# Kernel optimization log

Hardware: AMD Instinct MI355X
Metric: run time of the kernel (lower is better)

## Reference

```python
import jax, jax.numpy as jnp
import numpy as np
from jax.scipy.special import logsumexp

D_MODEL = 512
NHEAD = 8
BATCH = 2
SEQ = 1024


def _safe_log_relu(v):
    # log(max(v, 0)) with well-defined (zero) gradient where v <= 0
    pos = v > 0
    return jnp.where(pos, jnp.log(jnp.where(pos, v, 1.0)), -jnp.inf)


def _split_heads(t, h):
    b, l, hd = t.shape
    return t.reshape(b, l, h, hd // h).transpose(0, 2, 1, 3)  # (B,H,L,d)


def setup_inputs() -> dict:
    key = jax.random.key(0)
    ks = jax.random.split(key, 9)
    s = 1.0 / np.sqrt(D_MODEL)
    x = jax.random.normal(ks[0], (BATCH, SEQ, D_MODEL), jnp.float32)
    mk = lambda k: jax.random.normal(k, (D_MODEL, D_MODEL), jnp.float32) * s
    mb = lambda k: jax.random.normal(k, (D_MODEL,), jnp.float32) * 0.02
    return {
        "x": x,
        "W_Q": mk(ks[1]), "b_Q": mb(ks[2]),
        "W_K": mk(ks[3]), "b_K": mb(ks[4]),
        "W_V": mk(ks[5]), "b_V": mb(ks[6]),
        "W_O": mk(ks[7]), "b_O": mb(ks[8]),
    }


def reference(x, W_Q, b_Q, W_K, b_K, W_V, b_V, W_O, b_O):
    # self-attention: queries = keys = values = x
    Q = _split_heads(x @ W_Q.T + b_Q, NHEAD)  # (B,H,L,D)
    K = _split_heads(x @ W_K.T + b_K, NHEAD)  # (B,H,L,D)
    V = _split_heads(x @ W_V.T + b_V, NHEAD)  # (B,H,L,Dv)

    # normalizer: log sum_j sum_d exp(Q_id) * exp(K_jd)
    log_B = logsumexp(Q + logsumexp(K, axis=-2, keepdims=True), axis=-1)  # (B,H,L)

    log_V_plus = _safe_log_relu(V)[..., None, :]    # (B,H,L,1,Dv)
    log_V_minus = _safe_log_relu(-V)[..., None, :]  # (B,H,L,1,Dv)

    # reduce over key positions: (B,H,L,D,Dv) -> (B,H,D,Dv)
    lse_KV_plus = logsumexp(K[..., :, :, None] + log_V_plus, axis=-3)
    lse_KV_minus = logsumexp(K[..., :, :, None] + log_V_minus, axis=-3)

    # reduce over feature dim D: (B,H,L,D,Dv) -> (B,H,L,Dv)
    log_A_plus = logsumexp(Q[..., None] + lse_KV_plus[..., None, :, :], axis=-2)
    log_A_minus = logsumexp(Q[..., None] + lse_KV_minus[..., None, :, :], axis=-2)

    heads = jnp.exp(log_A_plus - log_B[..., None]) - jnp.exp(log_A_minus - log_B[..., None])

    b, h, l, dv = heads.shape
    joined = heads.transpose(0, 2, 1, 3).reshape(b, l, h * dv)
    return joined @ W_O.T + b_O
```

## Files before the change

### kernel.cpp

```cpp
#include <hip/hip_runtime.h>
#include <math.h>

#define DM   512
#define NH   8
#define HD   64
#define B_   2
#define L_   1024
#define M_   (B_ * L_)

typedef __attribute__((ext_vector_type(8))) short  bfrag;
typedef __attribute__((ext_vector_type(4))) float  fv4;
typedef __attribute__((ext_vector_type(4))) unsigned short usv4;
typedef __attribute__((ext_vector_type(8))) unsigned short usv8;

__device__ __forceinline__ unsigned short f32_bf16_rne(float f) {
    unsigned u = __float_as_uint(f);
    unsigned r = u + 0x7FFF + ((u >> 16) & 1);
    return (unsigned short)(r >> 16);
}
__device__ __forceinline__ float bf16_f32(unsigned short h) {
    return __uint_as_float(((unsigned)h) << 16);
}

__device__ __forceinline__ void cvt8(const float4 a, const float4 b,
                                     usv8* hi, usv8* lo) {
    float f[8] = {a.x, a.y, a.z, a.w, b.x, b.y, b.z, b.w};
#pragma unroll
    for (int k = 0; k < 8; ++k) {
        unsigned short h = f32_bf16_rne(f[k]);
        (*hi)[k] = h;
        (*lo)[k] = f32_bf16_rne(f[k] - bf16_f32(h));
    }
}

__device__ __forceinline__ void stage16(const unsigned short* g, unsigned short* l) {
    __builtin_amdgcn_global_load_lds(
        (const __attribute__((address_space(1))) void*)g,
        (__attribute__((address_space(3))) void*)l,
        16, 0, 0);
}

#define TM 64
#define TN 64
#define TK 32
#define LDA 32
#define NSTEP (DM / TK)

__global__ __launch_bounds__(256) void gemm_qkv_kernel(
    const float* __restrict__ x,
    const float* __restrict__ Wq, const float* __restrict__ Wk,
    const float* __restrict__ Wv,
    const float* __restrict__ bq, const float* __restrict__ bk,
    const float* __restrict__ bv,
    float* __restrict__ Qe, float* __restrict__ Ke, float* __restrict__ V,
    float* __restrict__ zred) {
    __shared__ __align__(16) unsigned short Ah[2][TM * LDA];
    __shared__ __align__(16) unsigned short Al[2][TM * LDA];
    __shared__ __align__(16) unsigned short Bh[2][TN * LDA];
    __shared__ __align__(16) unsigned short Bl[2][TN * LDA];

    const int z = blockIdx.z;
    const float* W    = (z == 0) ? Wq : (z == 1) ? Wk : Wv;
    const float* bias = (z == 0) ? bq : (z == 1) ? bk : bv;
    float* C          = (z == 0) ? Qe : (z == 1) ? Ke : V;
    const int m0 = blockIdx.y * TM, n0 = blockIdx.x * TN;
    const int do_exp = (z < 2);

    const int tid = threadIdx.x;
    if (blockIdx.x == 0 && blockIdx.y == 0 && z == 0) {
        float4 zv = {0.f, 0.f, 0.f, 0.f};
        *(float4*)(zred + (size_t)tid * 4) = zv;
    }

    const int wave = tid >> 6, lane = tid & 63;
    const int quad = lane >> 4, r16 = lane & 15;
    const int srow = lane >> 2;
    const int scol = (lane & 3) << 3;
    const size_t gaBase = (size_t)(m0 + wave * 16 + srow) * DM + scol;
    const size_t gbBase = (size_t)(n0 + wave * 16 + srow) * DM + scol;
    const int soff = (wave * 16 + srow) * LDA + scol;

    fv4 acc[4] = {};

    {
        float4 a0 = *(const float4*)(x + gaBase);
        float4 a1 = *(const float4*)(x + gaBase + 4);
        float4 b0 = *(const float4*)(W + gbBase);
        float4 b1 = *(const float4*)(W + gbBase + 4);
        usv8 h, l;
        cvt8(a0, a1, &h, &l);
        *(usv8*)(&Ah[0][soff]) = h; *(usv8*)(&Al[0][soff]) = l;
        cvt8(b0, b1, &h, &l);
        *(usv8*)(&Bh[0][soff]) = h; *(usv8*)(&Bl[0][soff]) = l;
    }
    __syncthreads();

    int cur = 0;
    for (int t = 0; t < NSTEP; ++t) {
        float4 na0, na1, nb0, nb1;
        if (t + 1 < NSTEP) {
            const size_t k = (size_t)(t + 1) * TK;
            na0 = *(const float4*)(x + gaBase + k);
            na1 = *(const float4*)(x + gaBase + k + 4);
            nb0 = *(const float4*)(W + gbBase + k);
            nb1 = *(const float4*)(W + gbBase + k + 4);
        }
        const int aoff = (wave * 16 + r16) * LDA + quad * 8;
        bfrag ah = *(const bfrag*)(&Ah[cur][aoff]);
        bfrag al = *(const bfrag*)(&Al[cur][aoff]);
        bfrag bh[4], bl[4];
#pragma unroll
        for (int j = 0; j < 4; ++j) {
            const int boff = (j * 16 + r16) * LDA + quad * 8;
            bh[j] = *(const bfrag*)(&Bh[cur][boff]);
            bl[j] = *(const bfrag*)(&Bl[cur][boff]);
        }
#pragma unroll
        for (int j = 0; j < 4; ++j) {
            acc[j] = __builtin_amdgcn_mfma_f32_16x16x32_bf16(ah, bh[j], acc[j], 0, 0, 0);
            acc[j] = __builtin_amdgcn_mfma_f32_16x16x32_bf16(ah, bl[j], acc[j], 0, 0, 0);
            acc[j] = __builtin_amdgcn_mfma_f32_16x16x32_bf16(al, bh[j], acc[j], 0, 0, 0);
        }
        if (t + 1 < NSTEP) {
            usv8 h, l;
            cvt8(na0, na1, &h, &l);
            *(usv8*)(&Ah[cur ^ 1][soff]) = h; *(usv8*)(&Al[cur ^ 1][soff]) = l;
            cvt8(nb0, nb1, &h, &l);
            *(usv8*)(&Bh[cur ^ 1][soff]) = h; *(usv8*)(&Bl[cur ^ 1][soff]) = l;
        }
        __syncthreads();
        cur ^= 1;
    }

#pragma unroll
    for (int j = 0; j < 4; ++j) {
        int n = n0 + j * 16 + r16;
        float bn = bias[n];
#pragma unroll
        for (int r = 0; r < 4; ++r) {
            int m = m0 + wave * 16 + quad * 4 + r;
            float v = acc[j][r] + bn;
            if (do_exp) v = __expf(v);
            C[(size_t)m * DM + n] = v;
        }
    }
}

__global__ __launch_bounds__(256) void gemm_out_kernel(
    const unsigned short* __restrict__ jh, const unsigned short* __restrict__ jl,
    const unsigned short* __restrict__ w2h, const unsigned short* __restrict__ w2l,
    const float* __restrict__ bo, float* __restrict__ C) {
    __shared__ __align__(16) unsigned short Ah[2][TM * LDA];
    __shared__ __align__(16) unsigned short Al[2][TM * LDA];
    __shared__ __align__(16) unsigned short Bh[2][TN * LDA];
    __shared__ __align__(16) unsigned short Bl[2][TN * LDA];

    const int bb = blockIdx.y >> 4;
    const unsigned short* Ahg = jh;
    const unsigned short* Alg = jl;
    const unsigned short* Bhg = w2h + (size_t)bb * 262144;
    const unsigned short* Blg = w2l + (size_t)bb * 262144;
    const int m0 = blockIdx.y * TM, n0 = blockIdx.x * TN;

    const int tid  = threadIdx.x;
    const int wave = tid >> 6, lane = tid & 63;
    const int quad = lane >> 4, r16 = lane & 15;
    const int srow = lane >> 2;
    const int scol = (lane & 3) << 3;
    const size_t gaBase = (size_t)(m0 + wave * 16 + srow) * DM + scol;
    const size_t gbBase = (size_t)(n0 + wave * 16 + srow) * DM + scol;
    const int ldst = wave * 512;

    fv4 acc[4] = {};

    stage16(Ahg + gaBase, &Ah[0][ldst]);
    stage16(Alg + gaBase, &Al[0][ldst]);
    stage16(Bhg + gbBase, &Bh[0][ldst]);
    stage16(Blg + gbBase, &Bl[0][ldst]);
    __syncthreads();

    int cur = 0;
    for (int t = 0; t < NSTEP; ++t) {
        if (t + 1 < NSTEP) {
            const size_t koff = (size_t)(t + 1) * TK;
            stage16(Ahg + gaBase + koff, &Ah[cur ^ 1][ldst]);
            stage16(Alg + gaBase + koff, &Al[cur ^ 1][ldst]);
            stage16(Bhg + gbBase + koff, &Bh[cur ^ 1][ldst]);
            stage16(Blg + gbBase + koff, &Bl[cur ^ 1][ldst]);
        }
        const int aoff = (wave * 16 + r16) * LDA + quad * 8;
        bfrag ah = *(const bfrag*)(&Ah[cur][aoff]);
        bfrag al = *(const bfrag*)(&Al[cur][aoff]);
        bfrag bh[4], bl[4];
#pragma unroll
        for (int j = 0; j < 4; ++j) {
            const int boff = (j * 16 + r16) * LDA + quad * 8;
            bh[j] = *(const bfrag*)(&Bh[cur][boff]);
            bl[j] = *(const bfrag*)(&Bl[cur][boff]);
        }
#pragma unroll
        for (int j = 0; j < 4; ++j) {
            acc[j] = __builtin_amdgcn_mfma_f32_16x16x32_bf16(ah, bh[j], acc[j], 0, 0, 0);
            acc[j] = __builtin_amdgcn_mfma_f32_16x16x32_bf16(ah, bl[j], acc[j], 0, 0, 0);
            acc[j] = __builtin_amdgcn_mfma_f32_16x16x32_bf16(al, bh[j], acc[j], 0, 0, 0);
        }
        __syncthreads();
        cur ^= 1;
    }

#pragma unroll
    for (int j = 0; j < 4; ++j) {
        int n = n0 + j * 16 + r16;
        float bn = bo[n];
#pragma unroll
        for (int r = 0; r < 4; ++r) {
            int m = m0 + wave * 16 + quad * 4 + r;
            C[(size_t)m * DM + n] = acc[j][r] + bn;
        }
    }
}

#define JT 64
__global__ __launch_bounds__(256) void kv_stats_kernel(
    const float* __restrict__ Kbuf, const float* __restrict__ Vbuf,
    float* __restrict__ Spart, float* __restrict__ zred) {
    const int split = blockIdx.x, bh = blockIdx.y;
    const int b = bh >> 3, h = bh & 7;
    const int j0 = split * JT;

    __shared__ __align__(16) float EK[JT][HD + 4];
    __shared__ __align__(16) float VS[JT][HD + 4];

    const int tid = threadIdx.x;
#pragma unroll
    for (int t = 0; t < 4; ++t) {
        int idx = tid + t * 256;
        int r = idx >> 4;
        int c = (idx & 15) << 2;
        size_t row = (size_t)(b * L_ + j0 + r) * DM + h * HD + c;
        *(float4*)&EK[r][c] = *(const float4*)(Kbuf + row);
        *(float4*)&VS[r][c] = *(const float4*)(Vbuf + row);
    }
    __syncthreads();

    const int tx = tid & 15, ty = tid >> 4;
    float acc[4][4] = {{0.f}};
#pragma unroll 8
    for (int jj = 0; jj < JT; ++jj) {
        float4 ek = *(const float4*)&EK[jj][ty * 4];
        float4 vs = *(const float4*)&VS[jj][tx * 4];
        float e[4] = {ek.x, ek.y, ek.z, ek.w};
        float v[4] = {vs.x, vs.y, vs.z, vs.w};
#pragma unroll
        for (int i = 0; i < 4; ++i)
#pragma unroll
            for (int j = 0; j < 4; ++j) acc[i][j] += e[i] * v[j];
    }

    float* sp = Spart + ((size_t)bh * 16 + split) * (HD * HD);
#pragma unroll
    for (int i = 0; i < 4; ++i) {
        float4 o; o.x = acc[i][0]; o.y = acc[i][1]; o.z = acc[i][2]; o.w = acc[i][3];
        *(float4*)(sp + (ty * 4 + i) * HD + tx * 4) = o;
    }
    if (tid < HD) {
        float z = 0.f;
#pragma unroll 8
        for (int jj = 0; jj < JT; ++jj) z += EK[jj][tid];
        atomicAdd(zred + (size_t)bh * HD + tid, z);
    }
}

__global__ __launch_bounds__(256) void mid_kernel(
    const float* __restrict__ Spart, const float* __restrict__ zred,
    const float* __restrict__ Qbuf, const float* __restrict__ Wo,
    unsigned short* __restrict__ w2h, unsigned short* __restrict__ w2l,
    unsigned short* __restrict__ jh, unsigned short* __restrict__ jl) {
    const int tid = threadIdx.x;
    const int bid = blockIdx.x;
    if (bid < 128) {
        __shared__ __align__(16) float Sl[HD][HD + 4];
        __shared__ __align__(16) float Wol[HD][HD + 4];
        const int b = bid >> 6, r = bid & 63;
        const int h = r >> 3, nq = r & 7;
        const int n0 = nq * 64, bh = b * NH + h;
        const float* sp = Spart + (size_t)bh * 16 * (HD * HD);
#pragma unroll
        for (int t4 = 0; t4 < 4; ++t4) {
            int idx4 = tid + t4 * 256;
            const float* p0 = sp + (size_t)idx4 * 4;
            float4 s = {0.f, 0.f, 0.f, 0.f};
#pragma unroll
            for (int p = 0; p < 16; ++p) {
                float4 v = *(const float4*)(p0 + (size_t)p * (HD * HD));
                s.x += v.x; s.y += v.y; s.z += v.z; s.w += v.w;
            }
            int d = idx4 >> 4, e4 = (idx4 & 15) << 2;
            *(float4*)&Sl[d][e4] = s;
            *(float4*)&Wol[d][e4] =
                *(const float4*)(Wo + (size_t)(n0 + d) * DM + h * HD + e4);
        }
        __syncthreads();
        const int nl = tid & 15;
        const int d0 = tid >> 4;
        float acc[4][4] = {};
#pragma unroll
        for (int e4 = 0; e4 < 16; ++e4) {
            float4 w[4], s[4];
#pragma unroll
            for (int j = 0; j < 4; ++j) w[j] = *(const float4*)&Wol[nl + j * 16][e4 * 4];
#pragma unroll
            for (int i = 0; i < 4; ++i) s[i] = *(const float4*)&Sl[d0 + i * 16][e4 * 4];
#pragma unroll
            for (int j = 0; j < 4; ++j)
#pragma unroll
                for (int i = 0; i < 4; ++i)
                    acc[j][i] += w[j].x * s[i].x + w[j].y * s[i].y
                               + w[j].z * s[i].z + w[j].w * s[i].w;
        }
#pragma unroll
        for (int j = 0; j < 4; ++j) {
            int n = n0 + nl + j * 16;
#pragma unroll
            for (int i = 0; i < 4; ++i) {
                int d = d0 + i * 16;
                size_t addr = ((size_t)(b * DM + n)) * DM + h * HD + d;
                float v = acc[j][i];
                unsigned short hh = f32_bf16_rne(v);
                w2h[addr] = hh;
                w2l[addr] = f32_bf16_rne(v - bf16_f32(hh));
            }
        }
    } else {
        const int bid2 = bid - 128;
        const int w = tid >> 6, lane = tid & 63;
        const int b = bid2 >> 5;
        const int row0 = bid2 * 32 + w * 8;
        const float4 z0 = *(const float4*)(zred + (size_t)b * DM + lane * 8);
        const float4 z1 = *(const float4*)(zred + (size_t)b * DM + lane * 8 + 4);
#pragma unroll
        for (int rr = 0; rr < 8; ++rr) {
            const size_t rowoff = (size_t)(row0 + rr) * DM + lane * 8;
            float4 q0 = *(const float4*)(Qbuf + rowoff);
            float4 q1 = *(const float4*)(Qbuf + rowoff + 4);
            float part = q0.x * z0.x + q0.y * z0.y + q0.z * z0.z + q0.w * z0.w
                       + q1.x * z1.x + q1.y * z1.y + q1.z * z1.z + q1.w * z1.w;
            part += __shfl_xor(part, 1, 64);
            part += __shfl_xor(part, 2, 64);
            part += __shfl_xor(part, 4, 64);
            float inv = 1.0f / part;
            float v[8] = {q0.x * inv, q0.y * inv, q0.z * inv, q0.w * inv,
                          q1.x * inv, q1.y * inv, q1.z * inv, q1.w * inv};
            usv8 hv, lv;
#pragma unroll
            for (int k = 0; k < 8; ++k) {
                unsigned short hh = f32_bf16_rne(v[k]);
                hv[k] = hh;
                lv[k] = f32_bf16_rne(v[k] - bf16_f32(hh));
            }
            *(usv8*)(jh + rowoff) = hv;
            *(usv8*)(jl + rowoff) = lv;
        }
    }
}

extern "C" void kernel_launch(void* const* d_in, const int* in_sizes, int n_in,
                              void* d_out, int out_size, void* d_ws, size_t ws_size,
                              hipStream_t stream) {
    const float* x  = (const float*)d_in[0];
    const float* Wq = (const float*)d_in[1];
    const float* bq = (const float*)d_in[2];
    const float* Wk = (const float*)d_in[3];
    const float* bk = (const float*)d_in[4];
    const float* Wv = (const float*)d_in[5];
    const float* bv = (const float*)d_in[6];
    const float* Wo = (const float*)d_in[7];
    const float* bo = (const float*)d_in[8];
    float* out = (float*)d_out;

    float* f = (float*)d_ws;
    const size_t NQ = (size_t)M_ * DM;
    float* Qe    = f;
    float* Ke    = f + NQ;
    float* V     = f + 2 * NQ;
    float* Spart = f + 3 * NQ;
    float* zred  = f + 4 * NQ;
    unsigned short* u = (unsigned short*)(f + 4 * NQ + 1024);
    unsigned short* jh  = u;
    unsigned short* jl  = jh + NQ;
    unsigned short* w2h = jl + NQ;
    unsigned short* w2l = w2h + 524288;

    dim3 gQKV(DM / TN, M_ / TM, 3);
    gemm_qkv_kernel<<<gQKV, 256, 0, stream>>>(x, Wq, Wk, Wv, bq, bk, bv,
                                              Qe, Ke, V, zred);

    kv_stats_kernel<<<dim3(16, 16), 256, 0, stream>>>(Ke, V, Spart, zred);

    mid_kernel<<<192, 256, 0, stream>>>(Spart, zred, Qe, Wo, w2h, w2l, jh, jl);

    dim3 gO(DM / TN, M_ / TM, 1);
    gemm_out_kernel<<<gO, 256, 0, stream>>>(jh, jl, w2h, w2l, bo, out);
}
```

Baseline: 131.3 us.

## Fuse K column-sum into QKV GEMM epilogue and regroup middle kernels

The K column sums (zred) are now accumulated in the QKV GEMM epilogue through shared-memory and global atomics, so the stats kernel no longer reduces them. That lets the Q normalization and bf16 split move into the same launch as the K^T V partial products (kv_scale_kernel), while the Wo fold becomes its own kernel. Zeroing zred moves to a hipMemsetAsync. The aim is to shorten the critical path by running the Q scaling alongside the KV stats, at the cost of extra atomics in the GEMM epilogue and one more launch (the memset).

```diff
diff --git a/kernel.cpp b/kernel.cpp
--- a/kernel.cpp
+++ b/kernel.cpp
@@ -58,6 +58,7 @@
     __shared__ __align__(16) unsigned short Al[2][TM * LDA];
     __shared__ __align__(16) unsigned short Bh[2][TN * LDA];
     __shared__ __align__(16) unsigned short Bl[2][TN * LDA];
+    __shared__ float zl[TN];
 
     const int z = blockIdx.z;
     const float* W    = (z == 0) ? Wq : (z == 1) ? Wk : Wv;
@@ -65,13 +66,9 @@
     float* C          = (z == 0) ? Qe : (z == 1) ? Ke : V;
     const int m0 = blockIdx.y * TM, n0 = blockIdx.x * TN;
     const int do_exp = (z < 2);
-
-    const int tid = threadIdx.x;
-    if (blockIdx.x == 0 && blockIdx.y == 0 && z == 0) {
-        float4 zv = {0.f, 0.f, 0.f, 0.f};
-        *(float4*)(zred + (size_t)tid * 4) = zv;
-    }
-
+    const int do_z   = (z == 1);
+
+    const int tid  = threadIdx.x;
     const int wave = tid >> 6, lane = tid & 63;
     const int quad = lane >> 4, r16 = lane & 15;
     const int srow = lane >> 2;
@@ -79,6 +76,8 @@
     const size_t gaBase = (size_t)(m0 + wave * 16 + srow) * DM + scol;
     const size_t gbBase = (size_t)(n0 + wave * 16 + srow) * DM + scol;
     const int soff = (wave * 16 + srow) * LDA + scol;
+
+    if (do_z && tid < TN) zl[tid] = 0.f;
 
     fv4 acc[4] = {};
 
@@ -136,203 +135,74 @@
     for (int j = 0; j < 4; ++j) {
         int n = n0 + j * 16 + r16;
         float bn = bias[n];
+        float cs = 0.f;
 #pragma unroll
         for (int r = 0; r < 4; ++r) {
             int m = m0 + wave * 16 + quad * 4 + r;
             float v = acc[j][r] + bn;
             if (do_exp) v = __expf(v);
             C[(size_t)m * DM + n] = v;
-        }
-    }
-}
-
-__global__ __launch_bounds__(256) void gemm_out_kernel(
-    const unsigned short* __restrict__ jh, const unsigned short* __restrict__ jl,
-    const unsigned short* __restrict__ w2h, const unsigned short* __restrict__ w2l,
-    const float* __restrict__ bo, float* __restrict__ C) {
-    __shared__ __align__(16) unsigned short Ah[2][TM * LDA];
-    __shared__ __align__(16) unsigned short Al[2][TM * LDA];
-    __shared__ __align__(16) unsigned short Bh[2][TN * LDA];
-    __shared__ __align__(16) unsigned short Bl[2][TN * LDA];
-
-    const int bb = blockIdx.y >> 4;
-    const unsigned short* Ahg = jh;
-    const unsigned short* Alg = jl;
-    const unsigned short* Bhg = w2h + (size_t)bb * 262144;
-    const unsigned short* Blg = w2l + (size_t)bb * 262144;
-    const int m0 = blockIdx.y * TM, n0 = blockIdx.x * TN;
-
-    const int tid  = threadIdx.x;
-    const int wave = tid >> 6, lane = tid & 63;
-    const int quad = lane >> 4, r16 = lane & 15;
-    const int srow = lane >> 2;
-    const int scol = (lane & 3) << 3;
-    const size_t gaBase = (size_t)(m0 + wave * 16 + srow) * DM + scol;
-    const size_t gbBase = (size_t)(n0 + wave * 16 + srow) * DM + scol;
-    const int ldst = wave * 512;
-
-    fv4 acc[4] = {};
-
-    stage16(Ahg + gaBase, &Ah[0][ldst]);
-    stage16(Alg + gaBase, &Al[0][ldst]);
-    stage16(Bhg + gbBase, &Bh[0][ldst]);
-    stage16(Blg + gbBase, &Bl[0][ldst]);
-    __syncthreads();
-
-    int cur = 0;
-    for (int t = 0; t < NSTEP; ++t) {
-        if (t + 1 < NSTEP) {
-            const size_t koff = (size_t)(t + 1) * TK;
-            stage16(Ahg + gaBase + koff, &Ah[cur ^ 1][ldst]);
-            stage16(Alg + gaBase + koff, &Al[cur ^ 1][ldst]);
-            stage16(Bhg + gbBase + koff, &Bh[cur ^ 1][ldst]);
-            stage16(Blg + gbBase + koff, &Bl[cur ^ 1][ldst]);
-        }
-        const int aoff = (wave * 16 + r16) * LDA + quad * 8;
-        bfrag ah = *(const bfrag*)(&Ah[cur][aoff]);
-        bfrag al = *(const bfrag*)(&Al[cur][aoff]);
-        bfrag bh[4], bl[4];
-#pragma unroll
-        for (int j = 0; j < 4; ++j) {
-            const int boff = (j * 16 + r16) * LDA + quad * 8;
-            bh[j] = *(const bfrag*)(&Bh[cur][boff]);
-            bl[j] = *(const bfrag*)(&Bl[cur][boff]);
-        }
-#pragma unroll
-        for (int j = 0; j < 4; ++j) {
-            acc[j] = __builtin_amdgcn_mfma_f32_16x16x32_bf16(ah, bh[j], acc[j], 0, 0, 0);
-            acc[j] = __builtin_amdgcn_mfma_f32_16x16x32_bf16(ah, bl[j], acc[j], 0, 0, 0);
-            acc[j] = __builtin_amdgcn_mfma_f32_16x16x32_bf16(al, bh[j], acc[j], 0, 0, 0);
-        }
+            cs += v;
+        }
+        if (do_z) atomicAdd(&zl[j * 16 + r16], cs);
+    }
+    if (do_z) {
         __syncthreads();
-        cur ^= 1;
-    }
-
-#pragma unroll
-    for (int j = 0; j < 4; ++j) {
-        int n = n0 + j * 16 + r16;
-        float bn = bo[n];
-#pragma unroll
-        for (int r = 0; r < 4; ++r) {
-            int m = m0 + wave * 16 + quad * 4 + r;
-            C[(size_t)m * DM + n] = acc[j][r] + bn;
+        if (tid < TN) {
+            const int b = blockIdx.y >> 4;
+            atomicAdd(zred + (size_t)b * DM + n0 + tid, zl[tid]);
         }
     }
 }
 
 #define JT 64
-__global__ __launch_bounds__(256) void kv_stats_kernel(
+__global__ __launch_bounds__(256) void kv_scale_kernel(
     const float* __restrict__ Kbuf, const float* __restrict__ Vbuf,
-    float* __restrict__ Spart, float* __restrict__ zred) {
-    const int split = blockIdx.x, bh = blockIdx.y;
-    const int b = bh >> 3, h = bh & 7;
-    const int j0 = split * JT;
-
-    __shared__ __align__(16) float EK[JT][HD + 4];
-    __shared__ __align__(16) float VS[JT][HD + 4];
-
+    const float* __restrict__ Qbuf, const float* __restrict__ zred,
+    float* __restrict__ Spart,
+    unsigned short* __restrict__ jh, unsigned short* __restrict__ jl) {
+    const int id  = blockIdx.x;
     const int tid = threadIdx.x;
-#pragma unroll
-    for (int t = 0; t < 4; ++t) {
-        int idx = tid + t * 256;
-        int r = idx >> 4;
-        int c = (idx & 15) << 2;
-        size_t row = (size_t)(b * L_ + j0 + r) * DM + h * HD + c;
-        *(float4*)&EK[r][c] = *(const float4*)(Kbuf + row);
-        *(float4*)&VS[r][c] = *(const float4*)(Vbuf + row);
-    }
-    __syncthreads();
-
-    const int tx = tid & 15, ty = tid >> 4;
-    float acc[4][4] = {{0.f}};
+    if (id < 256) {
+        const int split = id & 15, bh = id >> 4;
+        const int b = bh >> 3, h = bh & 7;
+        const int j0 = split * JT;
+
+        __shared__ __align__(16) float EK[JT][HD + 4];
+        __shared__ __align__(16) float VS[JT][HD + 4];
+#pragma unroll
+        for (int t = 0; t < 4; ++t) {
+            int idx = tid + t * 256;
+            int r = idx >> 4;
+            int c = (idx & 15) << 2;
+            size_t row = (size_t)(b * L_ + j0 + r) * DM + h * HD + c;
+            *(float4*)&EK[r][c] = *(const float4*)(Kbuf + row);
+            *(float4*)&VS[r][c] = *(const float4*)(Vbuf + row);
+        }
+        __syncthreads();
+
+        const int tx = tid & 15, ty = tid >> 4;
+        float acc[4][4] = {{0.f}};
 #pragma unroll 8
-    for (int jj = 0; jj < JT; ++jj) {
-        float4 ek = *(const float4*)&EK[jj][ty * 4];
-        float4 vs = *(const float4*)&VS[jj][tx * 4];
-        float e[4] = {ek.x, ek.y, ek.z, ek.w};
-        float v[4] = {vs.x, vs.y, vs.z, vs.w};
-#pragma unroll
-        for (int i = 0; i < 4; ++i)
-#pragma unroll
-            for (int j = 0; j < 4; ++j) acc[i][j] += e[i] * v[j];
-    }
-
-    float* sp = Spart + ((size_t)bh * 16 + split) * (HD * HD);
-#pragma unroll
-    for (int i = 0; i < 4; ++i) {
-        float4 o; o.x = acc[i][0]; o.y = acc[i][1]; o.z = acc[i][2]; o.w = acc[i][3];
-        *(float4*)(sp + (ty * 4 + i) * HD + tx * 4) = o;
-    }
-    if (tid < HD) {
-        float z = 0.f;
-#pragma unroll 8
-        for (int jj = 0; jj < JT; ++jj) z += EK[jj][tid];
-        atomicAdd(zred + (size_t)bh * HD + tid, z);
-    }
-}
-
-__global__ __launch_bounds__(256) void mid_kernel(
-    const float* __restrict__ Spart, const float* __restrict__ zred,
-    const float* __restrict__ Qbuf, const float* __restrict__ Wo,
-    unsigned short* __restrict__ w2h, unsigned short* __restrict__ w2l,
-    unsigned short* __restrict__ jh, unsigned short* __restrict__ jl) {
-    const int tid = threadIdx.x;
-    const int bid = blockIdx.x;
-    if (bid < 128) {
-        __shared__ __align__(16) float Sl[HD][HD + 4];
-        __shared__ __align__(16) float Wol[HD][HD + 4];
-        const int b = bid >> 6, r = bid & 63;
-        const int h = r >> 3, nq = r & 7;
-        const int n0 = nq * 64, bh = b * NH + h;
-        const float* sp = Spart + (size_t)bh * 16 * (HD * HD);
-#pragma unroll
-        for (int t4 = 0; t4 < 4; ++t4) {
-            int idx4 = tid + t4 * 256;
-            const float* p0 = sp + (size_t)idx4 * 4;
-            float4 s = {0.f, 0.f, 0.f, 0.f};
-#pragma unroll
-            for (int p = 0; p < 16; ++p) {
-                float4 v = *(const float4*)(p0 + (size_t)p * (HD * HD));
-                s.x += v.x; s.y += v.y; s.z += v.z; s.w += v.w;
-            }
-            int d = idx4 >> 4, e4 = (idx4 & 15) << 2;
-            *(float4*)&Sl[d][e4] = s;
-            *(float4*)&Wol[d][e4] =
-                *(const float4*)(Wo + (size_t)(n0 + d) * DM + h * HD + e4);
-        }
-        __syncthreads();
-        const int nl = tid & 15;
-        const int d0 = tid >> 4;
-        float acc[4][4] = {};
-#pragma unroll
-        for (int e4 = 0; e4 < 16; ++e4) {
-            float4 w[4], s[4];
-#pragma unroll
-            for (int j = 0; j < 4; ++j) w[j] = *(const float4*)&Wol[nl + j * 16][e4 * 4];
-#pragma unroll
-            for (int i = 0; i < 4; ++i) s[i] = *(const float4*)&Sl[d0 + i * 16][e4 * 4];
-#pragma unroll
-            for (int j = 0; j < 4; ++j)
-#pragma unroll
-                for (int i = 0; i < 4; ++i)
-                    acc[j][i] += w[j].x * s[i].x + w[j].y * s[i].y
-                               + w[j].z * s[i].z + w[j].w * s[i].w;
-        }
-#pragma unroll
-        for (int j = 0; j < 4; ++j) {
-            int n = n0 + nl + j * 16;
-#pragma unroll
-            for (int i = 0; i < 4; ++i) {
-                int d = d0 + i * 16;
-                size_t addr = ((size_t)(b * DM + n)) * DM + h * HD + d;
-                float v = acc[j][i];
-                unsigned short hh = f32_bf16_rne(v);
-                w2h[addr] = hh;
-                w2l[addr] = f32_bf16_rne(v - bf16_f32(hh));
-            }
+        for (int jj = 0; jj < JT; ++jj) {
+            float4 ek = *(const float4*)&EK[jj][ty * 4];
+            float4 vs = *(const float4*)&VS[jj][tx * 4];
+            float e[4] = {ek.x, ek.y, ek.z, ek.w};
+            float v[4] = {vs.x, vs.y, vs.z, vs.w};
+#pragma unroll
+            for (int i = 0; i < 4; ++i)
+#pragma unroll
+                for (int j = 0; j < 4; ++j) acc[i][j] += e[i] * v[j];
+        }
+
+        float* sp = Spart + ((size_t)bh * 16 + split) * (HD * HD);
+#pragma unroll
+        for (int i = 0; i < 4; ++i) {
+            float4 o; o.x = acc[i][0]; o.y = acc[i][1]; o.z = acc[i][2]; o.w = acc[i][3];
+            *(float4*)(sp + (ty * 4 + i) * HD + tx * 4) = o;
         }
     } else {
-        const int bid2 = bid - 128;
+        const int bid2 = id - 256;
         const int w = tid >> 6, lane = tid & 63;
         const int b = bid2 >> 5;
         const int row0 = bid2 * 32 + w * 8;
@@ -364,6 +234,139 @@
     }
 }
 
+__global__ __launch_bounds__(256) void fold_kernel(
+    const float* __restrict__ Spart, const float* __restrict__ Wo,
+    unsigned short* __restrict__ w2h, unsigned short* __restrict__ w2l) {
+    const int tid = threadIdx.x;
+    const int bid = blockIdx.x;
+    __shared__ __align__(16) float Sl[HD][HD + 4];
+    __shared__ __align__(16) float Wol[HD][HD + 4];
+    const int b = bid >> 6, r = bid & 63;
+    const int h = r >> 3, nq = r & 7;
+    const int n0 = nq * 64, bh = b * NH + h;
+    const float* sp = Spart + (size_t)bh * 16 * (HD * HD);
+#pragma unroll
+    for (int t4 = 0; t4 < 4; ++t4) {
+        int idx4 = tid + t4 * 256;
+        const float* p0 = sp + (size_t)idx4 * 4;
+        float4 s = {0.f, 0.f, 0.f, 0.f};
+#pragma unroll
+        for (int p = 0; p < 16; ++p) {
+            float4 v = *(const float4*)(p0 + (size_t)p * (HD * HD));
+            s.x += v.x; s.y += v.y; s.z += v.z; s.w += v.w;
+        }
+        int d = idx4 >> 4, e4 = (idx4 & 15) << 2;
+        *(float4*)&Sl[d][e4] = s;
+        *(float4*)&Wol[d][e4] =
+            *(const float4*)(Wo + (size_t)(n0 + d) * DM + h * HD + e4);
+    }
+    __syncthreads();
+    const int nl = tid & 15;
+    const int d0 = tid >> 4;
+    float acc[4][4] = {};
+#pragma unroll
+    for (int e4 = 0; e4 < 16; ++e4) {
+        float4 w[4], s[4];
+#pragma unroll
+        for (int j = 0; j < 4; ++j) w[j] = *(const float4*)&Wol[nl + j * 16][e4 * 4];
+#pragma unroll
+        for (int i = 0; i < 4; ++i) s[i] = *(const float4*)&Sl[d0 + i * 16][e4 * 4];
+#pragma unroll
+        for (int j = 0; j < 4; ++j)
+#pragma unroll
+            for (int i = 0; i < 4; ++i)
+                acc[j][i] += w[j].x * s[i].x + w[j].y * s[i].y
+                           + w[j].z * s[i].z + w[j].w * s[i].w;
+    }
+#pragma unroll
+    for (int j = 0; j < 4; ++j) {
+        int n = n0 + nl + j * 16;
+#pragma unroll
+        for (int i = 0; i < 4; ++i) {
+            int d = d0 + i * 16;
+            size_t addr = ((size_t)(b * DM + n)) * DM + h * HD + d;
+            float v = acc[j][i];
+            unsigned short hh = f32_bf16_rne(v);
+            w2h[addr] = hh;
+            w2l[addr] = f32_bf16_rne(v - bf16_f32(hh));
+        }
+    }
+}
+
+__global__ __launch_bounds__(256) void gemm_out_kernel(
+    const unsigned short* __restrict__ jh, const unsigned short* __restrict__ jl,
+    const unsigned short* __restrict__ w2h, const unsigned short* __restrict__ w2l,
+    const float* __restrict__ bo, float* __restrict__ C) {
+    __shared__ __align__(16) unsigned short Ah[2][TM * LDA];
+    __shared__ __align__(16) unsigned short Al[2][TM * LDA];
+    __shared__ __align__(16) unsigned short Bh[2][TN * LDA];
+    __shared__ __align__(16) unsigned short Bl[2][TN * LDA];
+
+    const int bb = blockIdx.y >> 4;
+    const unsigned short* Ahg = jh;
+    const unsigned short* Alg = jl;
+    const unsigned short* Bhg = w2h + (size_t)bb * 262144;
+    const unsigned short* Blg = w2l + (size_t)bb * 262144;
+    const int m0 = blockIdx.y * TM, n0 = blockIdx.x * TN;
+
+    const int tid  = threadIdx.x;
+    const int wave = tid >> 6, lane = tid & 63;
+    const int quad = lane >> 4, r16 = lane & 15;
+    const int srow = lane >> 2;
+    const int scol = (lane & 3) << 3;
+    const size_t gaBase = (size_t)(m0 + wave * 16 + srow) * DM + scol;
+    const size_t gbBase = (size_t)(n0 + wave * 16 + srow) * DM + scol;
+    const int ldst = wave * 512;
+
+    fv4 acc[4] = {};
+
+    stage16(Ahg + gaBase, &Ah[0][ldst]);
+    stage16(Alg + gaBase, &Al[0][ldst]);
+    stage16(Bhg + gbBase, &Bh[0][ldst]);
+    stage16(Blg + gbBase, &Bl[0][ldst]);
+    __syncthreads();
+
+    int cur = 0;
+    for (int t = 0; t < NSTEP; ++t) {
+        if (t + 1 < NSTEP) {
+            const size_t koff = (size_t)(t + 1) * TK;
+            stage16(Ahg + gaBase + koff, &Ah[cur ^ 1][ldst]);
+            stage16(Alg + gaBase + koff, &Al[cur ^ 1][ldst]);
+            stage16(Bhg + gbBase + koff, &Bh[cur ^ 1][ldst]);
+            stage16(Blg + gbBase + koff, &Bl[cur ^ 1][ldst]);
+        }
+        const int aoff = (wave * 16 + r16) * LDA + quad * 8;
+        bfrag ah = *(const bfrag*)(&Ah[cur][aoff]);
+        bfrag al = *(const bfrag*)(&Al[cur][aoff]);
+        bfrag bh[4], bl[4];
+#pragma unroll
+        for (int j = 0; j < 4; ++j) {
+            const int boff = (j * 16 + r16) * LDA + quad * 8;
+            bh[j] = *(const bfrag*)(&Bh[cur][boff]);
+            bl[j] = *(const bfrag*)(&Bl[cur][boff]);
+        }
+#pragma unroll
+        for (int j = 0; j < 4; ++j) {
+            acc[j] = __builtin_amdgcn_mfma_f32_16x16x32_bf16(ah, bh[j], acc[j], 0, 0, 0);
+            acc[j] = __builtin_amdgcn_mfma_f32_16x16x32_bf16(ah, bl[j], acc[j], 0, 0, 0);
+            acc[j] = __builtin_amdgcn_mfma_f32_16x16x32_bf16(al, bh[j], acc[j], 0, 0, 0);
+        }
+        __syncthreads();
+        cur ^= 1;
+    }
+
+#pragma unroll
+    for (int j = 0; j < 4; ++j) {
+        int n = n0 + j * 16 + r16;
+        float bn = bo[n];
+#pragma unroll
+        for (int r = 0; r < 4; ++r) {
+            int m = m0 + wave * 16 + quad * 4 + r;
+            C[(size_t)m * DM + n] = acc[j][r] + bn;
+        }
+    }
+}
+
 extern "C" void kernel_launch(void* const* d_in, const int* in_sizes, int n_in,
                               void* d_out, int out_size, void* d_ws, size_t ws_size,
                               hipStream_t stream) {
@@ -391,13 +394,15 @@
     unsigned short* w2h = jl + NQ;
     unsigned short* w2l = w2h + 524288;
 
+    hipMemsetAsync((void*)zred, 0, 1024 * sizeof(float), stream);
+
     dim3 gQKV(DM / TN, M_ / TM, 3);
     gemm_qkv_kernel<<<gQKV, 256, 0, stream>>>(x, Wq, Wk, Wv, bq, bk, bv,
                                               Qe, Ke, V, zred);
 
-    kv_stats_kernel<<<dim3(16, 16), 256, 0, stream>>>(Ke, V, Spart, zred);
-
-    mid_kernel<<<192, 256, 0, stream>>>(Spart, zred, Qe, Wo, w2h, w2l, jh, jl);
+    kv_scale_kernel<<<320, 256, 0, stream>>>(Ke, V, Qe, zred, Spart, jh, jl);
+
+    fold_kernel<<<128, 256, 0, stream>>>(Spart, Wo, w2h, w2l);
 
     dim3 gO(DM / TN, M_ / TM, 1);
     gemm_out_kernel<<<gO, 256, 0, stream>>>(jh, jl, w2h, w2l, bo, out);
```

Measured after the change: 134.1 us. 2.2% more time.
